# Kernel optimization log

Hardware: AMD Instinct MI355X
Metric: run time of the kernel (lower is better)

## Reference

```python
import jax, jax.numpy as jnp
import numpy as np

ALPHA = 0.1  # init kwarg alpha


def setup_inputs() -> dict:
    key = jax.random.key(0)
    k1, k2 = jax.random.split(key)
    x = jax.random.normal(k1, (32, 192, 64, 64), dtype=jnp.float32)
    delta = jax.random.normal(k2, (32, 1, 64, 64), dtype=jnp.float32)
    return {"x_bchw": x, "delta": delta}


def reference(x_bchw, delta):
    # Faithful fixed-shape version of LayerTokenPrune.forward.
    # Kept tokens are stream-compacted to the front (stable, preserving
    # original token order, matching torch.where index order); dropped
    # positions are zero-padded, matching the zero-pad in the original.
    B, C, H, W = x_bchw.shape
    L = H * W
    tok = jnp.transpose(x_bchw, (0, 2, 3, 1)).reshape(B, L, C)  # [B, L, C]

    delta_tok = delta.reshape(B, -1)  # 4-dim delta branch -> [B, L]
    imp = jnp.abs(delta_tok)
    lo = imp.min(axis=1, keepdims=True)
    hi = imp.max(axis=1, keepdims=True)
    rng = jnp.maximum(hi - lo, 1e-3)  # clamp_min(0.001)
    imp = (imp - lo) / rng

    mu = imp.mean(axis=1, keepdims=True)
    sigma = imp.std(axis=1, keepdims=True, ddof=1)  # torch std is unbiased
    theta = mu - ALPHA * sigma
    keep = imp >= theta  # [B, L] bool; max-imp token always kept (theta<=mu<=1)

    # Stable compaction: kept token indices first, in original order.
    # jnp.argsort is stable, so sorting the key (0 for keep, 1 for drop)
    # reproduces torch.where's ascending-index order for kept tokens.
    order = jnp.argsort(jnp.logical_not(keep).astype(jnp.int32), axis=1)  # [B, L]
    gathered = jnp.take_along_axis(tok, order[:, :, None], axis=1)  # [B, L, C]

    counts = keep.sum(axis=1)  # [B]
    valid = (jnp.arange(L)[None, :] < counts[:, None]).astype(tok.dtype)  # [B, L]
    tok_new = gathered * valid[:, :, None]  # zero out pad positions

    # Fixed-shape analogue of the sqrt reshape: pad to full L = H*W grid.
    y = tok_new.reshape(B, H, W, C).transpose(0, 3, 1, 2)  # [B, C, H, W]

    keep_ratio = counts.astype(jnp.float32).mean() / L
    theta_mean = theta.mean()
    return y, keep_ratio, theta_mean
```

## Files before the change

### kernel.cpp

```cpp
#include <hip/hip_runtime.h>
#include <math.h>

#define B_ 32
#define C_ 192
#define H_ 64
#define W_ 64
#define L_ 4096
#define L4_ 1024
#define NTHREADS 256
#define PER_THREAD 16

typedef float  f32x4 __attribute__((ext_vector_type(4)));

__global__ __launch_bounds__(NTHREADS) void stats_scan_kernel(
    const float* __restrict__ delta,
    int*  __restrict__ src_idx,
    int*  __restrict__ counts,
    float* __restrict__ thetas)
{
  const int b = blockIdx.x;
  const int t = threadIdx.x;
  const int lane = t & 63;
  const int wid  = t >> 6;

  __shared__ float  smin[4], smax[4];
  __shared__ float  s_lo, s_rng, s_theta;
  __shared__ double dsum[4], dsum2[4];
  __shared__ int    wsum[4];

  const float* dp = delta + (size_t)b * L_;

  float a[PER_THREAD];
  const float4* d4 = (const float4*)dp;
  #pragma unroll
  for (int i = 0; i < 4; ++i) {
    float4 v = d4[t * 4 + i];
    a[i*4+0] = fabsf(v.x); a[i*4+1] = fabsf(v.y);
    a[i*4+2] = fabsf(v.z); a[i*4+3] = fabsf(v.w);
  }

  float lmin = a[0], lmax = a[0];
  #pragma unroll
  for (int i = 1; i < PER_THREAD; ++i) {
    lmin = fminf(lmin, a[i]);
    lmax = fmaxf(lmax, a[i]);
  }
  #pragma unroll
  for (int off = 32; off; off >>= 1) {
    lmin = fminf(lmin, __shfl_down(lmin, off, 64));
    lmax = fmaxf(lmax, __shfl_down(lmax, off, 64));
  }
  if (lane == 0) { smin[wid] = lmin; smax[wid] = lmax; }
  __syncthreads();
  if (t == 0) {
    float lo = fminf(fminf(smin[0], smin[1]), fminf(smin[2], smin[3]));
    float hi = fmaxf(fmaxf(smax[0], smax[1]), fmaxf(smax[2], smax[3]));
    s_lo  = lo;
    s_rng = fmaxf(hi - lo, 1e-3f);
  }
  __syncthreads();
  const float lo  = s_lo;
  const float rng = s_rng;

  double s = 0.0, s2 = 0.0;
  #pragma unroll
  for (int i = 0; i < PER_THREAD; ++i) {
    float imp = (a[i] - lo) / rng;
    a[i] = imp;
    s  += (double)imp;
    s2 += (double)imp * (double)imp;
  }
  #pragma unroll
  for (int off = 32; off; off >>= 1) {
    s  += __shfl_down(s,  off, 64);
    s2 += __shfl_down(s2, off, 64);
  }
  if (lane == 0) { dsum[wid] = s; dsum2[wid] = s2; }
  __syncthreads();
  if (t == 0) {
    double S  = dsum[0]  + dsum[1]  + dsum[2]  + dsum[3];
    double S2 = dsum2[0] + dsum2[1] + dsum2[2] + dsum2[3];
    double mu  = S / (double)L_;
    double var = (S2 - S * S / (double)L_) / (double)(L_ - 1);
    if (var < 0.0) var = 0.0;
    double sigma = sqrt(var);
    s_theta = (float)(mu - 0.1 * sigma);
  }
  __syncthreads();
  const float theta = s_theta;

  int flags = 0, cnt = 0;
  #pragma unroll
  for (int i = 0; i < PER_THREAD; ++i) {
    int k = (a[i] >= theta) ? 1 : 0;
    cnt += k;
    flags |= (k << i);
  }
  int inc = cnt;
  #pragma unroll
  for (int off = 1; off < 64; off <<= 1) {
    int y = __shfl_up(inc, off, 64);
    if (lane >= off) inc += y;
  }
  if (lane == 63) wsum[wid] = inc;
  __syncthreads();
  int base = inc - cnt;
  #pragma unroll
  for (int w = 0; w < 4; ++w)
    if (w < wid) base += wsum[w];

  int* sb = src_idx + (size_t)b * L_;
  int p = base;
  #pragma unroll
  for (int i = 0; i < PER_THREAD; ++i) {
    if ((flags >> i) & 1) { sb[p++] = t * PER_THREAD + i; }
  }
  if (t == NTHREADS - 1) {
    counts[b] = base + cnt;
    thetas[b] = theta;
  }
}

__global__ __launch_bounds__(NTHREADS) void gather_kernel(
    const float* __restrict__ x,
    const int*  __restrict__ src_idx,
    const int*  __restrict__ counts,
    const float* __restrict__ thetas,
    float* __restrict__ out,
    float* __restrict__ out_tail)
{
  const int bc = blockIdx.x;
  const int b  = bc / C_;
  const int t  = threadIdx.x;

  if (bc == 0 && t < 64) {
    float cc = (t < B_) ? (float)counts[t] : 0.0f;
    float th = (t < B_) ? thetas[t]        : 0.0f;
    #pragma unroll
    for (int off = 32; off; off >>= 1) {
      cc += __shfl_down(cc, off, 64);
      th += __shfl_down(th, off, 64);
    }
    if (t == 0) {
      out_tail[0] = (cc / (float)B_) / (float)L_;
      out_tail[1] = th / (float)B_;
    }
  }

  const size_t rowbase = (size_t)bc * L_;
  const float* xr  = x + rowbase;
  const int    cnt = counts[b];
  const int4*  s4b = (const int4*)(src_idx + (size_t)b * L_);
  f32x4*       o4  = (f32x4*)(out + rowbase);

  #pragma unroll
  for (int i = 0; i < 4; ++i) {
    const int j  = t + NTHREADS * i;
    const int d0 = j * 4;
    f32x4 r = {0.0f, 0.0f, 0.0f, 0.0f};
    if (d0 < cnt) {
      const int4 s = s4b[j];
      r.x = xr[s.x & (L_ - 1)];
      r.y = (d0 + 1 < cnt) ? xr[s.y & (L_ - 1)] : 0.0f;
      r.z = (d0 + 2 < cnt) ? xr[s.z & (L_ - 1)] : 0.0f;
      r.w = (d0 + 3 < cnt) ? xr[s.w & (L_ - 1)] : 0.0f;
    }
    o4[j] = r;
  }
}

extern "C" void kernel_launch(void* const* d_in, const int* in_sizes, int n_in,
                              void* d_out, int out_size, void* d_ws, size_t ws_size,
                              hipStream_t stream) {
  const float* x     = (const float*)d_in[0];
  const float* delta = (const float*)d_in[1];
  float* out = (float*)d_out;

  int*   src_idx = (int*)d_ws;
  int*   counts  = (int*)((char*)d_ws + (size_t)B_ * L_ * 4);
  float* thetas  = (float*)((char*)d_ws + (size_t)B_ * L_ * 4 + 128);

  const size_t y_elems = (size_t)B_ * C_ * L_;
  float* out_tail = out + y_elems;

  stats_scan_kernel<<<B_, NTHREADS, 0, stream>>>(delta, src_idx, counts, thetas);
  gather_kernel<<<B_ * C_, NTHREADS, 0, stream>>>(x, src_idx, counts, thetas,
                                                  out, out_tail);
}
```

Before: 190.7 us.

## Split gather into multi-row index-reuse kernel and direct kernel over batch halves

The gather is split across two launches. The first half of the batches runs in a kernel that loads the compaction indices into registers once and reuses them across four channel rows per block. The second half keeps the original one-row-per-block kernel. The aim is to cut repeated index loads and per-block overhead for part of the work, at the cost of an extra launch and fewer, heavier blocks for the first half.

After: 194.2 us. Within noise of the previous version (+1.9%).

```diff
diff --git a/kernel.cpp b/kernel.cpp
--- a/kernel.cpp
+++ b/kernel.cpp
@@ -9,6 +9,8 @@
 #define L4_ 1024
 #define NTHREADS 256
 #define PER_THREAD 16
+#define ROWS_DEEP 4
+#define BHALF 16
 
 typedef float  f32x4 __attribute__((ext_vector_type(4)));
 
@@ -121,7 +123,7 @@
   }
 }
 
-__global__ __launch_bounds__(NTHREADS) void gather_kernel(
+__global__ __launch_bounds__(NTHREADS) void gather_deep(
     const float* __restrict__ x,
     const int*  __restrict__ src_idx,
     const int*  __restrict__ counts,
@@ -129,11 +131,12 @@
     float* __restrict__ out,
     float* __restrict__ out_tail)
 {
-  const int bc = blockIdx.x;
-  const int b  = bc / C_;
-  const int t  = threadIdx.x;
-
-  if (bc == 0 && t < 64) {
+  const int blk = blockIdx.x;
+  const int bc0 = blk * ROWS_DEEP;
+  const int b   = bc0 / C_;
+  const int t   = threadIdx.x;
+
+  if (blk == 0 && t < 64) {
     float cc = (t < B_) ? (float)counts[t] : 0.0f;
     float th = (t < B_) ? thetas[t]        : 0.0f;
     #pragma unroll
@@ -146,6 +149,51 @@
       out_tail[1] = th / (float)B_;
     }
   }
+
+  const int cnt = counts[b];
+
+  int sidx[PER_THREAD];
+  {
+    const int4* s4b = (const int4*)(src_idx + (size_t)b * L_);
+    #pragma unroll
+    for (int i = 0; i < 4; ++i) {
+      const int4 s = s4b[t + NTHREADS * i];
+      sidx[i*4+0] = s.x & (L_ - 1);
+      sidx[i*4+1] = s.y & (L_ - 1);
+      sidx[i*4+2] = s.z & (L_ - 1);
+      sidx[i*4+3] = s.w & (L_ - 1);
+    }
+  }
+
+  #pragma unroll
+  for (int r = 0; r < ROWS_DEEP; ++r) {
+    const float* xr = x   + (size_t)(bc0 + r) * L_;
+    f32x4*       o4 = (f32x4*)(out + (size_t)(bc0 + r) * L_);
+    #pragma unroll
+    for (int i = 0; i < 4; ++i) {
+      const int j  = t + NTHREADS * i;
+      const int d0 = j * 4;
+      f32x4 rr = {0.0f, 0.0f, 0.0f, 0.0f};
+      if (d0 < cnt) {
+        rr.x = xr[sidx[i*4+0]];
+        rr.y = (d0 + 1 < cnt) ? xr[sidx[i*4+1]] : 0.0f;
+        rr.z = (d0 + 2 < cnt) ? xr[sidx[i*4+2]] : 0.0f;
+        rr.w = (d0 + 3 < cnt) ? xr[sidx[i*4+3]] : 0.0f;
+      }
+      o4[j] = rr;
+    }
+  }
+}
+
+__global__ __launch_bounds__(NTHREADS) void gather_direct(
+    const float* __restrict__ x,
+    const int*  __restrict__ src_idx,
+    const int*  __restrict__ counts,
+    float* __restrict__ out)
+{
+  const int bc = BHALF * C_ + blockIdx.x;
+  const int b  = bc / C_;
+  const int t  = threadIdx.x;
 
   const size_t rowbase = (size_t)bc * L_;
   const float* xr  = x + rowbase;
@@ -184,6 +232,8 @@
   float* out_tail = out + y_elems;
 
   stats_scan_kernel<<<B_, NTHREADS, 0, stream>>>(delta, src_idx, counts, thetas);
-  gather_kernel<<<B_ * C_, NTHREADS, 0, stream>>>(x, src_idx, counts, thetas,
-                                                  out, out_tail);
-}
+
+  gather_deep<<<BHALF * C_ / ROWS_DEEP, NTHREADS, 0, stream>>>(
+      x, src_idx, counts, thetas, out, out_tail);
+  gather_direct<<<BHALF * C_, NTHREADS, 0, stream>>>(x, src_idx, counts, out);
+}
```

## Warp-specialize gather into producer/consumer pipeline through LDS ring buffer

Applied to the files above, without the earlier changes.

The gather kernel now handles 8 channels per block. Two producer waves stream each x row into a 3-slot shared-memory ring with coalesced float4 loads. Two consumer waves gather from LDS using source indices and keep-masks loaded once per block, then write the output. Spin-wait flags on volatile shared memory replace per-row random global reads and amortize the index loads. The cost is fewer blocks, about 48KB of LDS per block, and possible stalls or correctness risk from the hand-rolled synchronization.

New measurement: 190.6 us. No clear change (-0.0%).

```diff
diff --git a/kernel.cpp b/kernel.cpp
--- a/kernel.cpp
+++ b/kernel.cpp
@@ -6,9 +6,10 @@
 #define H_ 64
 #define W_ 64
 #define L_ 4096
-#define L4_ 1024
 #define NTHREADS 256
 #define PER_THREAD 16
+#define CPB 8
+#define SLOTS 3
 
 typedef float  f32x4 __attribute__((ext_vector_type(4)));
 
@@ -121,7 +122,7 @@
   }
 }
 
-__global__ __launch_bounds__(NTHREADS) void gather_kernel(
+__global__ __launch_bounds__(NTHREADS) void gather_pc(
     const float* __restrict__ x,
     const int*  __restrict__ src_idx,
     const int*  __restrict__ counts,
@@ -129,11 +130,23 @@
     float* __restrict__ out,
     float* __restrict__ out_tail)
 {
-  const int bc = blockIdx.x;
-  const int b  = bc / C_;
-  const int t  = threadIdx.x;
-
-  if (bc == 0 && t < 64) {
+  __shared__ float slotbuf[SLOTS][L_];
+  __shared__ volatile int ready[SLOTS][2];
+  __shared__ volatile int done_[SLOTS][2];
+
+  const int blk  = blockIdx.x;
+  const int bc0  = blk * CPB;
+  const int b    = bc0 / C_;
+  const int t    = threadIdx.x;
+  const int w    = t >> 6;
+  const int lane = t & 63;
+
+  if (t < SLOTS) {
+    ready[t][0] = -1;      ready[t][1] = -1;
+    done_[t][0] = t - SLOTS; done_[t][1] = t - SLOTS;
+  }
+
+  if (blk == 0 && t < 64) {
     float cc = (t < B_) ? (float)counts[t] : 0.0f;
     float th = (t < B_) ? thetas[t]        : 0.0f;
     #pragma unroll
@@ -147,25 +160,69 @@
     }
   }
 
-  const size_t rowbase = (size_t)bc * L_;
-  const float* xr  = x + rowbase;
-  const int    cnt = counts[b];
-  const int4*  s4b = (const int4*)(src_idx + (size_t)b * L_);
-  f32x4*       o4  = (f32x4*)(out + rowbase);
-
-  #pragma unroll
-  for (int i = 0; i < 4; ++i) {
-    const int j  = t + NTHREADS * i;
-    const int d0 = j * 4;
-    f32x4 r = {0.0f, 0.0f, 0.0f, 0.0f};
-    if (d0 < cnt) {
-      const int4 s = s4b[j];
-      r.x = xr[s.x & (L_ - 1)];
-      r.y = (d0 + 1 < cnt) ? xr[s.y & (L_ - 1)] : 0.0f;
-      r.z = (d0 + 2 < cnt) ? xr[s.z & (L_ - 1)] : 0.0f;
-      r.w = (d0 + 3 < cnt) ? xr[s.w & (L_ - 1)] : 0.0f;
-    }
-    o4[j] = r;
+  __syncthreads();
+
+  if (w < 2) {
+    const int base4 = w * 512 + lane;
+    #pragma unroll
+    for (int r = 0; r < CPB; ++r) {
+      const int s = r % SLOTS;
+      while (done_[s][0] < r - SLOTS || done_[s][1] < r - SLOTS)
+        __builtin_amdgcn_s_sleep(1);
+      asm volatile("" ::: "memory");
+      const float4* xr = (const float4*)(x + (size_t)(bc0 + r) * L_);
+      float4 st[8];
+      #pragma unroll
+      for (int i = 0; i < 8; ++i) st[i] = xr[base4 + 64 * i];
+      float4* dst = (float4*)&slotbuf[s][0];
+      #pragma unroll
+      for (int i = 0; i < 8; ++i) dst[base4 + 64 * i] = st[i];
+      asm volatile("s_waitcnt lgkmcnt(0)" ::: "memory");
+      if (lane == 0) ready[s][w] = r;
+    }
+  } else {
+    const int cw  = w - 2;
+    const int cnt = counts[b];
+
+    int sidx[32];
+    unsigned kmask = 0;
+    const int4* s4b = (const int4*)(src_idx + (size_t)b * L_);
+    #pragma unroll
+    for (int i = 0; i < 8; ++i) {
+      const int j  = cw * 512 + lane + 64 * i;
+      const int4 s4 = s4b[j];
+      sidx[i*4+0] = s4.x & (L_ - 1);
+      sidx[i*4+1] = s4.y & (L_ - 1);
+      sidx[i*4+2] = s4.z & (L_ - 1);
+      sidx[i*4+3] = s4.w & (L_ - 1);
+      const int d0 = j * 4;
+      kmask |= (d0     < cnt ? 1u : 0u) << (i*4+0);
+      kmask |= (d0 + 1 < cnt ? 1u : 0u) << (i*4+1);
+      kmask |= (d0 + 2 < cnt ? 1u : 0u) << (i*4+2);
+      kmask |= (d0 + 3 < cnt ? 1u : 0u) << (i*4+3);
+    }
+
+    #pragma unroll
+    for (int r = 0; r < CPB; ++r) {
+      const int s = r % SLOTS;
+      while (ready[s][0] < r || ready[s][1] < r)
+        __builtin_amdgcn_s_sleep(1);
+      asm volatile("" ::: "memory");
+      const float* row = &slotbuf[s][0];
+      f32x4* o4 = (f32x4*)(out + (size_t)(bc0 + r) * L_);
+      #pragma unroll
+      for (int i = 0; i < 8; ++i) {
+        const int j = cw * 512 + lane + 64 * i;
+        f32x4 rr;
+        rr.x = ((kmask >> (i*4+0)) & 1) ? row[sidx[i*4+0]] : 0.0f;
+        rr.y = ((kmask >> (i*4+1)) & 1) ? row[sidx[i*4+1]] : 0.0f;
+        rr.z = ((kmask >> (i*4+2)) & 1) ? row[sidx[i*4+2]] : 0.0f;
+        rr.w = ((kmask >> (i*4+3)) & 1) ? row[sidx[i*4+3]] : 0.0f;
+        o4[j] = rr;
+      }
+      asm volatile("s_waitcnt lgkmcnt(0)" ::: "memory");
+      if (lane == 0) done_[s][cw] = r;
+    }
   }
 }
 
@@ -184,6 +241,6 @@
   float* out_tail = out + y_elems;
 
   stats_scan_kernel<<<B_, NTHREADS, 0, stream>>>(delta, src_idx, counts, thetas);
-  gather_kernel<<<B_ * C_, NTHREADS, 0, stream>>>(x, src_idx, counts, thetas,
-                                                  out, out_tail);
+  gather_pc<<<B_ * C_ / CPB, NTHREADS, 0, stream>>>(x, src_idx, counts, thetas,
+                                                    out, out_tail);
 }
```
